# Kernel optimization log

Hardware: AMD Instinct MI355X
Metric: run time of the kernel (lower is better)

## Reference

```python
import jax, jax.numpy as jnp
import numpy as np

NUM_RADII, NUM_THETA = 3, 16
RADIUS = 40.0
DT = 0.1
RELU_SHIFT = 0.2
B, N, NB, T_ENC, OTHER_CH = 4, 512, 512, 16, 3


def _rot_mats():
    # bin-center angles of the num_theta angular bins
    t = (jnp.arange(NUM_THETA, dtype=jnp.float32) + 0.5) * (2.0 * jnp.pi / NUM_THETA) - jnp.pi
    c, s = jnp.cos(t), jnp.sin(t)
    return jnp.stack([jnp.stack([c, -s], -1), jnp.stack([s, c], -1)], -2)  # [T,2,2]


def _steer_kernel(W):
    # W: [R,T,O,I,2,2]; equivariant steering K[r,t] = R(theta_t) W[r,t] R(theta_t)^T
    Rm = _rot_mats()
    K = jnp.einsum('tab,rtoibc,tdc->rtoiad', Rm, W, Rm)
    return K.reshape(NUM_RADII * NUM_THETA, W.shape[2], W.shape[3], 2, 2)  # [K,O,I,2,2]


def _equi_conv(src_pos, qry_pos, feats, mask, W):
    # src_pos [B,S,2], qry_pos [B,Q,2], feats [B,S,I,2] vector features, mask [B,Q,S]
    rel = src_pos[:, None, :, :] - qry_pos[:, :, None, :]          # [B,Q,S,2]
    d2 = jnp.sum(rel * rel, -1)
    dist = jnp.sqrt(d2 + 1e-9)
    theta = jnp.arctan2(rel[..., 1], rel[..., 0])
    rb = jnp.clip((dist / RADIUS * NUM_RADII).astype(jnp.int32), 0, NUM_RADII - 1)
    tb = jnp.mod(jnp.floor((theta + jnp.pi) / (2.0 * jnp.pi) * NUM_THETA).astype(jnp.int32), NUM_THETA)
    kidx = rb * NUM_THETA + tb                                     # [B,Q,S] polar bin id
    win = jnp.maximum(1.0 - d2 / (RADIUS * RADIUS), 0.0) ** 3      # smooth radial window
    w = win * mask
    H = jax.nn.one_hot(kidx, NUM_RADII * NUM_THETA, dtype=feats.dtype) * w[..., None]  # [B,Q,S,K]
    M = jnp.einsum('bqsk,bsiv->bqkiv', H, feats)                   # bin-accumulated neighbor features
    K = _steer_kernel(W)
    return jnp.einsum('bqkiv,koiuv->bqou', M, K)                   # [B,Q,O,2]


def _equi_linear(f, A, Bm):
    # rotation-equivariant linear on vector channels: (a*I + b*J) per (out,in)
    Jf = jnp.stack([-f[..., 1], f[..., 0]], -1)
    return jnp.einsum('oi,bniv->bnov', A, f) + jnp.einsum('oi,bniv->bnov', Bm, Jf)


def _forward(p0_enc, v0_enc, p0, v0, a, other_feats, box, box_feats, fluid_mask, box_mask,
             W_cf, W_co, A_df, B_df, layer_params):
    # update_pos_vel
    v1 = v0 + DT * a
    p1 = p0 + DT * (v0 + v1) * 0.5
    # forward(): feats = cat(other_feats, v0_enc) on channel dim -2
    feats = jnp.concatenate([other_feats, v0_enc], -2)
    # compute_correction
    fluid_feats = jnp.concatenate([v1[:, :, None, :], feats], -2)  # [B,N,20,2]
    out_conv_fluid = _equi_conv(p1, p1, fluid_feats, fluid_mask, W_cf)
    out_dense_fluid = _equi_linear(fluid_feats, A_df, B_df)
    out_conv_obst = _equi_conv(box, p1, box_feats[:, :, None, :], box_mask, W_co)
    output = jnp.concatenate([out_conv_obst, out_conv_fluid, out_dense_fluid], -2)  # [B,N,48,2]
    for (Wc, Ad, Bd) in layer_params:
        mags = (jnp.sum(output * output, -1) + 1e-6)[..., None]
        in_feats = output / mags * jax.nn.relu(mags - RELU_SHIFT)
        oc = _equi_conv(p1, p1, in_feats, fluid_mask, Wc)
        od = _equi_linear(in_feats, Ad, Bd)
        if od.shape[-2] == output.shape[-2]:
            output = oc + od + output
        else:
            output = oc + od
    corr = output / 128.0                                          # [B,N,1,2]
    # apply_correction
    p_corrected = p1 + corr[..., 0, :]
    v_corrected = (p_corrected - p0) / DT
    return p_corrected, v_corrected


def setup_inputs():
    key = jax.random.key(0)
    ks = jax.random.split(key, 32)
    d = {}
    d['p0_enc'] = jax.random.normal(ks[0], (B, N, T_ENC, 2), jnp.float32)
    d['v0_enc'] = jax.random.normal(ks[1], (B, N, T_ENC, 2), jnp.float32)
    d['p0'] = jax.random.uniform(ks[2], (B, N, 2), jnp.float32) * 100.0
    d['v0'] = jax.random.normal(ks[3], (B, N, 2), jnp.float32)
    d['a'] = jax.random.normal(ks[4], (B, N, 2), jnp.float32)
    d['other_feats'] = jax.random.normal(ks[5], (B, N, OTHER_CH, 2), jnp.float32)
    d['box'] = jax.random.uniform(ks[6], (B, NB, 2), jnp.float32) * 100.0
    d['box_feats'] = jax.random.normal(ks[7], (B, NB, 2), jnp.float32)
    d['fluid_mask'] = (jax.random.uniform(ks[8], (B, N, N)) < 0.5).astype(jnp.float32)
    d['box_mask'] = (jax.random.uniform(ks[9], (B, N, NB)) < 0.5).astype(jnp.float32)
    sc = 0.05
    d['W_cf'] = sc * jax.random.normal(ks[10], (NUM_RADII, NUM_THETA, 16, 20, 2, 2), jnp.float32)
    d['W_co'] = sc * jax.random.normal(ks[11], (NUM_RADII, NUM_THETA, 16, 1, 2, 2), jnp.float32)
    d['A_df'] = sc * jax.random.normal(ks[12], (16, 20), jnp.float32)
    d['B_df'] = sc * jax.random.normal(ks[13], (16, 20), jnp.float32)
    chans = [(32, 48), (32, 32), (32, 32), (1, 32)]
    for i, (o, ci) in enumerate(chans, start=1):
        d['W_c%d' % i] = sc * jax.random.normal(ks[13 + 3 * i], (NUM_RADII, NUM_THETA, o, ci, 2, 2), jnp.float32)
        d['A_d%d' % i] = sc * jax.random.normal(ks[14 + 3 * i], (o, ci), jnp.float32)
        d['B_d%d' % i] = sc * jax.random.normal(ks[15 + 3 * i], (o, ci), jnp.float32)
    return d


def reference(p0_enc, v0_enc, p0, v0, a, other_feats, box, box_feats, fluid_mask, box_mask,
              W_cf, W_co, A_df, B_df, W_c1, A_d1, B_d1, W_c2, A_d2, B_d2,
              W_c3, A_d3, B_d3, W_c4, A_d4, B_d4):
    layer_params = [(W_c1, A_d1, B_d1), (W_c2, A_d2, B_d2), (W_c3, A_d3, B_d3), (W_c4, A_d4, B_d4)]
    return _forward(p0_enc, v0_enc, p0, v0, a, other_feats, box, box_feats, fluid_mask, box_mask,
                    W_cf, W_co, A_df, B_df, layer_params)
```

## Files before the change

### kernel.cpp

```cpp
#include <hip/hip_runtime.h>
#include <cstdint>
#include <cstddef>

#define PI_F 3.14159265358979323846f

constexpr int BB = 4, NN = 512, BN = 2048, NBIN = 48;

typedef __attribute__((ext_vector_type(8))) short v8s;
typedef __attribute__((ext_vector_type(4))) float v4f;

__device__ __forceinline__ unsigned short f2bf(float f) {
  unsigned u = __float_as_uint(f);
  unsigned r = (u + 0x7FFFu + ((u >> 16) & 1u)) >> 16;
  return (unsigned short)r;
}
__device__ __forceinline__ float bf2f(unsigned short s) {
  return __uint_as_float(((unsigned)s) << 16);
}

__device__ __forceinline__ void steer_f32(const float* __restrict__ W, float* __restrict__ K2,
                                          int O, int I, int Ipad, int idx, int total) {
  if (idx >= total) return;
  int i = idx % Ipad;
  int o = (idx / Ipad) % O;
  int k = idx / (Ipad * O);
  int CTc = O * 2;
  size_t r0 = (size_t)((k*Ipad + i)*2 + 0) * CTc + o*2;
  size_t r1 = r0 + CTc;
  if (i >= I) { K2[r0]=0.f; K2[r0+1]=0.f; K2[r1]=0.f; K2[r1+1]=0.f; return; }
  int tt = k % 16;
  float ang = (tt + 0.5f) * (2.0f * PI_F / 16.0f) - PI_F;
  float ct = cosf(ang), st = sinf(ang);
  const float* Wp = W + ((size_t)(k*O + o)*I + i) * 4;
  float w00 = Wp[0], w01 = Wp[1], w10 = Wp[2], w11 = Wp[3];
  float rw00 = ct*w00 - st*w10, rw01 = ct*w01 - st*w11;
  float rw10 = st*w00 + ct*w10, rw11 = st*w01 + ct*w11;
  K2[r0 + 0] = rw00*ct - rw01*st;
  K2[r0 + 1] = rw10*ct - rw11*st;
  K2[r1 + 0] = rw00*st + rw01*ct;
  K2[r1 + 1] = rw10*st + rw11*ct;
}

__device__ __forceinline__ void steer_bf16T(const float* __restrict__ W,
                                            unsigned short* __restrict__ K2T,
                                            int O, int I, int Ipad, int Kd,
                                            int idx, int total) {
  if (idx >= total) return;
  int i = idx % Ipad;
  int o = (idx / Ipad) % O;
  int k = idx / (Ipad * O);
  size_t c0 = (size_t)(o*2 + 0) * Kd + (k*Ipad + i)*2;
  size_t c1 = (size_t)(o*2 + 1) * Kd + (k*Ipad + i)*2;
  if (i >= I) { K2T[c0]=0; K2T[c0+1]=0; K2T[c1]=0; K2T[c1+1]=0; return; }
  int tt = k % 16;
  float ang = (tt + 0.5f) * (2.0f * PI_F / 16.0f) - PI_F;
  float ct = cosf(ang), st = sinf(ang);
  const float* Wp = W + ((size_t)(k*O + o)*I + i) * 4;
  float w00 = Wp[0], w01 = Wp[1], w10 = Wp[2], w11 = Wp[3];
  float rw00 = ct*w00 - st*w10, rw01 = ct*w01 - st*w11;
  float rw10 = st*w00 + ct*w10, rw11 = st*w01 + ct*w11;
  K2T[c0 + 0] = f2bf(rw00*ct - rw01*st);
  K2T[c0 + 1] = f2bf(rw00*st + rw01*ct);
  K2T[c1 + 0] = f2bf(rw10*ct - rw11*st);
  K2T[c1 + 1] = f2bf(rw10*st + rw11*ct);
}

__global__ __launch_bounds__(256) void setup_kernel(
    const float* __restrict__ p0, const float* __restrict__ v0,
    const float* __restrict__ a, const float* __restrict__ other,
    const float* __restrict__ v0enc, float* __restrict__ p1, float* __restrict__ F0,
    const float* Wcf, unsigned short* K2CF, const float* Wco, float* K2CO,
    const float* Wc1, unsigned short* K2C1, const float* Wc2, unsigned short* K2C2,
    const float* Wc3, unsigned short* K2C3, const float* Wc4, float* K2C4) {
  int blk = blockIdx.x;
  int t = threadIdx.x;
  if (blk < 8) {
    int n = blk * 256 + t;
    float p0x = p0[n*2], p0y = p0[n*2+1];
    float v0x = v0[n*2], v0y = v0[n*2+1];
    float ax = a[n*2],  ay = a[n*2+1];
    float v1x = v0x + 0.1f*ax, v1y = v0y + 0.1f*ay;
    p1[n*2]   = p0x + 0.1f*(v0x+v1x)*0.5f;
    p1[n*2+1] = p0y + 0.1f*(v0y+v1y)*0.5f;
    float* F = F0 + (size_t)n*48;
    F[0] = v1x; F[1] = v1y;
    for (int c = 0; c < 3; ++c) {
      F[2+c*2]   = other[(n*3+c)*2];
      F[2+c*2+1] = other[(n*3+c)*2+1];
    }
    for (int c = 0; c < 16; ++c) {
      F[8+c*2]   = v0enc[(n*16+c)*2];
      F[8+c*2+1] = v0enc[(n*16+c)*2+1];
    }
    for (int c = 40; c < 48; ++c) F[c] = 0.0f;
  } else if (blk < 80)  steer_bf16T(Wcf, K2CF, 16, 20, 24, 2304, (blk-8)*256 + t, 18432);
  else if (blk < 83)  steer_f32(Wco, K2CO, 16, 1, 1,   (blk-80)*256 + t, 768);
  else if (blk < 371) steer_bf16T(Wc1, K2C1, 32, 48, 48, 4608, (blk-83)*256 + t, 73728);
  else if (blk < 563) steer_bf16T(Wc2, K2C2, 32, 32, 32, 3072, (blk-371)*256 + t, 49152);
  else if (blk < 755) steer_bf16T(Wc3, K2C3, 32, 32, 32, 3072, (blk-563)*256 + t, 49152);
  else                steer_f32(Wc4, K2C4, 1, 32, 32,  (blk-755)*256 + t, 1536);
}

__global__ __launch_bounds__(256) void pairs_all(const float* __restrict__ qry,
                                                 const float* __restrict__ srcF,
                                                 const float* __restrict__ maskF,
                                                 float* __restrict__ wlF, int* __restrict__ plF,
                                                 int* __restrict__ cntF,
                                                 const float* __restrict__ srcO,
                                                 const float* __restrict__ maskO,
                                                 float* __restrict__ wlO, int* __restrict__ plO,
                                                 int* __restrict__ cntO) {
  __shared__ int hist[4][48];
  __shared__ int bstart[4][48];
  __shared__ int runc[4][48];
  bool isBox = blockIdx.x >= 512;
  int qblk = isBox ? (blockIdx.x - 512) : blockIdx.x;
  const float* src = isBox ? srcO : srcF;
  const float* mask = isBox ? maskO : maskF;
  float* wlist = isBox ? wlO : wlF;
  int* plist = isBox ? plO : plF;
  int* cnt = isBox ? cntO : cntF;

  int wv = threadIdx.x >> 6;
  int lane = threadIdx.x & 63;
  int q = qblk * 4 + wv;
  int b = q >> 9;
  float qx = qry[q*2], qy = qry[q*2+1];
  const float* sb = src + b*1024;
  const float* mb = mask + (size_t)q*512;
  float* wl = wlist + (size_t)q*512;
  int* pl = plist + (size_t)q*512;

  if (lane < 48) { hist[wv][lane] = 0; runc[wv][lane] = 0; }

  float wreg[8]; int kreg[8];
  unsigned char predreg[8];
  for (int ch = 0; ch < 8; ++ch) {
    int s = ch*64 + lane;
    float sx = sb[s*2], sy = sb[s*2+1];
    float rx = sx - qx, ry = sy - qy;
    float d2 = rx*rx + ry*ry;
    float m = mb[s];
    float wi = fmaxf(1.0f - d2 / 1600.0f, 0.0f);
    float w = wi*wi*wi*m;
    bool pred = w > 0.0f;
    int k = 63;
    if (pred) {
      float dist = sqrtf(d2 + 1e-9f);
      float theta = atan2f(ry, rx);
      int rb = (int)(dist / 40.0f * 3.0f);
      rb = rb > 2 ? 2 : rb;
      float u = (theta + PI_F) / (2.0f * PI_F) * 16.0f;
      int tb = ((int)floorf(u)) & 15;
      k = rb*16 + tb;
      atomicAdd(&hist[wv][k], 1);
    }
    wreg[ch] = w; kreg[ch] = k; predreg[ch] = pred ? 1 : 0;
  }
  int cntv = (lane < 48) ? hist[wv][lane] : 0;
  int sc = cntv;
  #pragma unroll
  for (int off = 1; off < 64; off <<= 1) {
    int o = __shfl_up(sc, off);
    if (lane >= off) sc += o;
  }
  if (lane < 48) bstart[wv][lane] = sc - cntv;
  if (lane == 47) cnt[q] = sc;

  for (int ch = 0; ch < 8; ++ch) {
    bool pred = predreg[ch] != 0;
    int k = kreg[ch];
    float w = wreg[ch];
    unsigned long long mEq = __ballot(pred);
    #pragma unroll
    for (int bit = 0; bit < 6; ++bit) {
      unsigned long long mbm = __ballot((k >> bit) & 1);
      mEq &= ((k >> bit) & 1) ? mbm : ~mbm;
    }
    int rank = __popcll(mEq & ((1ull<<lane)-1ull));
    int total = __popcll(mEq);
    if (pred) {
      int bs = bstart[wv][k];
      int rc = runc[wv][k];
      int pos = bs + rc + rank;
      int s = ch*64 + lane;
      wl[pos] = w;
      pl[pos] = (s<<6) | k;
      if (rank == total - 1) runc[wv][k] = rc + total;
    }
  }
}

template<int C2>
__device__ __forceinline__ void accum_loop(float* __restrict__ M, int sw, int c, int nnz,
    const float* __restrict__ wls, const int* __restrict__ pls,
    const float* __restrict__ fb) {
  if (nnz <= 0) return;
  constexpr int W = 16;
  float wA[W], fA[W]; int kA[W];
  #pragma unroll
  for (int j = 0; j < W; ++j) {
    bool v = j < nnz;
    float wv = v ? wls[j] : 0.0f;
    int p = v ? pls[j] : 47;
    wA[j] = wv; kA[j] = p & 63;
    fA[j] = fb[(p >> 6) * C2];
  }
  int kcur = -1;
  float acc = 0.0f;
  for (int base = 0; base < nnz; base += W) {
    float wB[W], fB[W]; int kB[W];
    if (base + W < nnz) {
      #pragma unroll
      for (int j = 0; j < W; ++j) {
        int idx = base + W + j;
        bool v = idx < nnz;
        float wv = v ? wls[idx] : 0.0f;
        int p = v ? pls[idx] : 47;
        wB[j] = wv; kB[j] = p & 63;
        fB[j] = fb[(size_t)(p >> 6) * C2];
      }
    }
    asm volatile("" ::: "memory");
    #pragma unroll
    for (int j = 0; j < W; ++j) {
      acc = (kA[j] == kcur ? acc : 0.0f) + wA[j] * fA[j];
      kcur = kA[j];
      M[(kcur * C2 + c) ^ sw] = acc;
    }
    #pragma unroll
    for (int j = 0; j < W; ++j) { wA[j] = wB[j]; kA[j] = kB[j]; fA[j] = fB[j]; }
  }
}

template<int QB, int TPB>
__device__ __forceinline__ void stage_lists(int q0, const int* __restrict__ csh,
    const float* __restrict__ wlist, const int* __restrict__ plist,
    float* __restrict__ wsh, int* __restrict__ psh) {
  const int t = threadIdx.x;
  for (int i = t; i < QB*128; i += TPB) {
    int qs = i >> 7, j = i & 127;
    if (j*4 < csh[qs]) {
      ((float4*)(wsh + qs*512))[j] = ((const float4*)(wlist + (size_t)(q0+qs)*512))[j];
      ((int4*)(psh + qs*512))[j]   = ((const int4*)(plist + (size_t)(q0+qs)*512))[j];
    }
  }
}

template<int C2, int QB, int TPB>
__global__ __launch_bounds__(TPB, 1) void accum4(const float* __restrict__ wlist,
                                                 const int* __restrict__ plist,
                                                 const int* __restrict__ cnt,
                                                 const float* __restrict__ feats,
                                                 unsigned short* __restrict__ Mout) {
  constexpr int Kd = NBIN * C2;
  static_assert(TPB == QB * C2, "TPB must equal QB*C2");
  __shared__ float Ml[QB * Kd];
  __shared__ float wsh[QB*512];
  __shared__ int   psh[QB*512];
  __shared__ int   csh[QB];
  const int t = threadIdx.x;
  const int q0 = blockIdx.x * QB;
  for (int i = t; i < QB*Kd; i += TPB) Ml[i] = 0.0f;
  if (t < QB) csh[t] = (q0 + t < BN) ? cnt[q0 + t] : 0;
  __syncthreads();
  stage_lists<QB, TPB>(q0, csh, wlist, plist, wsh, psh);
  __syncthreads();
  {
    const int ql = t / C2, c = t % C2;
    const int q = q0 + ql;
    accum_loop<C2>(Ml + ql*Kd, 0, c, csh[ql],
                   wsh + ql*512, psh + ql*512,
                   feats + (size_t)(q >> 9)*512*C2 + c);
  }
  __syncthreads();
  const int rows = (q0 + QB <= BN) ? QB : (BN - q0);
  unsigned* dst = (unsigned*)(Mout + (size_t)q0 * Kd);
  const float2* s2 = (const float2*)Ml;
  const int lim = rows * (Kd/2);
  for (int i = t; i < lim; i += TPB) {
    float2 v = s2[i];
    dst[i] = (unsigned)f2bf(v.x) | ((unsigned)f2bf(v.y) << 16);
  }
}

template<int CT>
__global__ __launch_bounds__(256) void gemm_mfma(const unsigned short* __restrict__ A,
                                                 const unsigned short* __restrict__ B,
                                                 float* __restrict__ G, int Kd, int kn) {
  const int lane = threadIdx.x & 63;
  const int w = threadIdx.x >> 6;
  const int mblk = blockIdx.x;
  const int ks = blockIdx.y * 4 + w;
  const int k0 = ks * kn;
  const int m = lane & 15, quad = lane >> 4;
  constexpr int NT = CT / 16;
  const unsigned short* Ar0 = A + (size_t)(mblk*32 + m) * Kd + k0 + quad*8;
  const unsigned short* Ar1 = Ar0 + (size_t)16 * Kd;
  const unsigned short* Bp[NT];
  #pragma unroll
  for (int nt = 0; nt < NT; ++nt)
    Bp[nt] = B + (size_t)(nt*16 + m) * Kd + k0 + quad*8;
  v4f acc[2][NT];
  #pragma unroll
  for (int mt = 0; mt < 2; ++mt)
    for (int nt = 0; nt < NT; ++nt)
      acc[mt][nt] = (v4f){0.0f, 0.0f, 0.0f, 0.0f};
  for (int kt = 0; kt < kn; kt += 32) {
    v8s a0 = *(const v8s*)(Ar0 + kt);
    v8s a1 = *(const v8s*)(Ar1 + kt);
    #pragma unroll
    for (int nt = 0; nt < NT; ++nt) {
      v8s bv = *(const v8s*)(Bp[nt] + kt);
      acc[0][nt] = __builtin_amdgcn_mfma_f32_16x16x32_bf16(a0, bv, acc[0][nt], 0, 0, 0);
      acc[1][nt] = __builtin_amdgcn_mfma_f32_16x16x32_bf16(a1, bv, acc[1][nt], 0, 0, 0);
    }
  }
  float* Gb = G + ((size_t)ks * BN + mblk*32) * CT;
  #pragma unroll
  for (int mt = 0; mt < 2; ++mt)
    for (int nt = 0; nt < NT; ++nt)
      for (int r = 0; r < 4; ++r)
        Gb[(mt*16 + quad*4 + r) * CT + nt*16 + m] = acc[mt][nt][r];
}

__global__ void epilogueL(const float* __restrict__ Gp, int SPLIT,
                          const float* __restrict__ inPrev, int I,
                          const float* __restrict__ Ad, const float* __restrict__ Bd,
                          const float* __restrict__ prevOut, int doRes,
                          float* __restrict__ outCur, float* __restrict__ inNext) {
  int idx = blockIdx.x * blockDim.x + threadIdx.x;
  if (idx >= BN*32) return;
  int o = idx % 32, q = idx / 32;
  float x = 0.0f, y = 0.0f;
  for (int sp = 0; sp < SPLIT; ++sp) {
    size_t base = ((size_t)sp*BN + q)*64 + o*2;
    x += Gp[base]; y += Gp[base+1];
  }
  const float* f = inPrev + (size_t)q * I * 2;
  for (int i = 0; i < I; ++i) {
    float fx = f[i*2], fy = f[i*2+1];
    float Av = Ad[o*I+i], Bv = Bd[o*I+i];
    x += Av*fx - Bv*fy;
    y += Av*fy + Bv*fx;
  }
  if (doRes) {
    x += prevOut[(size_t)idx*2];
    y += prevOut[(size_t)idx*2+1];
  }
  outCur[(size_t)idx*2]   = x;
  outCur[(size_t)idx*2+1] = y;
  float m = x*x + y*y + 1e-6f;
  float sc = fmaxf(m - 0.2f, 0.0f) / m;
  inNext[(size_t)idx*2]   = x * sc;
  inNext[(size_t)idx*2+1] = y * sc;
}

__global__ __launch_bounds__(256, 1) void fused_s0(
    const float* __restrict__ wlF, const int* __restrict__ plF, const int* __restrict__ cntF,
    const float* __restrict__ F0, const unsigned short* __restrict__ K2CF,
    const float* __restrict__ wlO, const int* __restrict__ plO, const int* __restrict__ cntO,
    const float* __restrict__ boxf, const float* __restrict__ K2CO,
    const float* __restrict__ Adf, const float* __restrict__ Bdf,
    float* __restrict__ in1) {
  constexpr int QB = 4;
  constexpr int Kd = 2304;
  constexpr int KW = 576;
  __shared__ float Ml[QB * Kd];
  __shared__ float Mo[QB * 96];
  __shared__ float red[4][QB * 32];
  __shared__ float wshF[QB*512];
  __shared__ int   pshF[QB*512];
  __shared__ float wshO[QB*512];
  __shared__ int   pshO[QB*512];
  __shared__ int cshF[QB];
  __shared__ int cshO[QB];
  const int t = threadIdx.x;
  const int q0 = blockIdx.x * QB;
  for (int i = t; i < QB*Kd; i += 256) Ml[i] = 0.0f;
  for (int i = t; i < QB*96; i += 256) Mo[i] = 0.0f;
  if (t < QB) cshF[t] = cntF[q0 + t];
  else if (t < 2*QB) cshO[t-QB] = cntO[q0 + t - QB];
  __syncthreads();
  for (int i = t; i < 2*QB*128; i += 256) {
    int half = i >> 9;
    int qs = (i >> 7) & (QB-1), j = i & 127;
    if (half == 0) {
      if (j*4 < cshF[qs]) {
        ((float4*)(wshF + qs*512))[j] = ((const float4*)(wlF + (size_t)(q0+qs)*512))[j];
        ((int4*)(pshF + qs*512))[j]   = ((const int4*)(plF + (size_t)(q0+qs)*512))[j];
      }
    } else {
      if (j*4 < cshO[qs]) {
        ((float4*)(wshO + qs*512))[j] = ((const float4*)(wlO + (size_t)(q0+qs)*512))[j];
        ((int4*)(pshO + qs*512))[j]   = ((const int4*)(plO + (size_t)(q0+qs)*512))[j];
      }
    }
  }
  __syncthreads();
  if (t < 192) {
    const int ql = t / 48, c = t % 48;
    const int q = q0 + ql;
    accum_loop<48>(Ml + ql*Kd, (ql & 3) << 2, c, cshF[ql],
                   wshF + ql*512, pshF + ql*512,
                   F0 + (size_t)(q >> 9)*512*48 + c);
  } else if (t < 200) {
    const int idx = t - 192;
    const int ql = idx >> 1, c = idx & 1;
    const int q = q0 + ql;
    accum_loop<2>(Mo + ql*96, 0, c, cshO[ql],
                  wshO + ql*512, pshO + ql*512,
                  boxf + (size_t)(q >> 9)*1024 + c);
  }
  __syncthreads();
  {
    const int lane = t & 63, w = t >> 6;
    const int m = lane & 15, quad = lane >> 4;
    const int ar = m & 3;
    const int sw = ar << 2;
    const float* Abase = Ml + ar * Kd;
    const int kb = w * KW + quad * 8;
    const unsigned short* Bb0 = K2CF + (size_t)m * Kd + kb;
    const unsigned short* Bb1 = K2CF + (size_t)(16 + m) * Kd + kb;
    v4f acc[2];
    acc[0] = (v4f){0,0,0,0}; acc[1] = (v4f){0,0,0,0};
    float4 a0c = *(const float4*)(Abase + (kb ^ sw));
    float4 a1c = *(const float4*)(Abase + ((kb + 4) ^ sw));
    v8s b0c = *(const v8s*)(Bb0);
    v8s b1c = *(const v8s*)(Bb1);
    for (int kt = 0; kt < KW; kt += 32) {
      float4 a0n, a1n; v8s b0n, b1n;
      if (kt + 32 < KW) {
        const int jn = kb + kt + 32;
        a0n = *(const float4*)(Abase + (jn ^ sw));
        a1n = *(const float4*)(Abase + ((jn + 4) ^ sw));
        b0n = *(const v8s*)(Bb0 + kt + 32);
        b1n = *(const v8s*)(Bb1 + kt + 32);
      }
      v8s av;
      av[0]=(short)f2bf(a0c.x); av[1]=(short)f2bf(a0c.y); av[2]=(short)f2bf(a0c.z); av[3]=(short)f2bf(a0c.w);
      av[4]=(short)f2bf(a1c.x); av[5]=(short)f2bf(a1c.y); av[6]=(short)f2bf(a1c.z); av[7]=(short)f2bf(a1c.w);
      acc[0] = __builtin_amdgcn_mfma_f32_16x16x32_bf16(av, b0c, acc[0], 0, 0, 0);
      acc[1] = __builtin_amdgcn_mfma_f32_16x16x32_bf16(av, b1c, acc[1], 0, 0, 0);
      a0c = a0n; a1c = a1n; b0c = b0n; b1c = b1n;
    }
    if (quad == 0) {
      #pragma unroll
      for (int nt = 0; nt < 2; ++nt)
        #pragma unroll
        for (int r = 0; r < 4; ++r)
          red[w][r*32 + nt*16 + m] = acc[nt][r];
    }
  }
  __syncthreads();
  if (t < 192) {
    const int ql = t / 48, ch = t % 48;
    const int q = q0 + ql;
    float x = 0.0f, y = 0.0f;
    if (ch < 16) {
      const float* Mq = Mo + ql*96;
      for (int j = 0; j < 96; ++j) {
        float mv = Mq[j];
        x += mv * K2CO[j*32 + ch*2];
        y += mv * K2CO[j*32 + ch*2 + 1];
      }
    } else if (ch < 32) {
      int o = ch - 16;
      x = red[0][ql*32+o*2] + red[1][ql*32+o*2] + red[2][ql*32+o*2] + red[3][ql*32+o*2];
      y = red[0][ql*32+o*2+1] + red[1][ql*32+o*2+1] + red[2][ql*32+o*2+1] + red[3][ql*32+o*2+1];
    } else {
      int o = ch - 32;
      const float* f = F0 + (size_t)q*48;
      for (int i = 0; i < 20; ++i) {
        float fx = f[i*2], fy = f[i*2+1];
        float Av = Adf[o*20+i], Bv = Bdf[o*20+i];
        x += Av*fx - Bv*fy;
        y += Av*fy + Bv*fx;
      }
    }
    float mm = x*x + y*y + 1e-6f;
    float sc = fmaxf(mm - 0.2f, 0.0f) / mm;
    size_t idx = (size_t)q*48 + ch;
    in1[idx*2]   = x * sc;
    in1[idx*2+1] = y * sc;
  }
}

template<int C2, int CT, int I, int QB>
__global__ __launch_bounds__(C2*QB, 1) void fused_layer(
    const float* __restrict__ wlist, const int* __restrict__ plist,
    const int* __restrict__ cnt, const float* __restrict__ feats,
    const unsigned short* __restrict__ K2T,
    const float* __restrict__ Ad, const float* __restrict__ Bd,
    const float* __restrict__ prevOut, int doRes,
    float* __restrict__ outCur, float* __restrict__ inNext) {
  constexpr int Kd = NBIN * C2;
  constexpr int TPB = C2 * QB;
  constexpr int NW = TPB / 64;
  constexpr int KW = Kd / NW;
  constexpr int NT = CT / 16;
  static_assert(KW % 32 == 0, "KW must be multiple of 32");
  __shared__ float Ml[QB * Kd];
  __shared__ float red[NW][QB * CT];
  __shared__ float wsh[QB*512];
  __shared__ int   psh[QB*512];
  __shared__ int csh[QB];
  const int t = threadIdx.x;
  const int q0 = blockIdx.x * QB;
  for (int i = t; i < QB*Kd; i += TPB) Ml[i] = 0.0f;
  if (t < QB) csh[t] = cnt[q0 + t];
  __syncthreads();
  stage_lists<QB, TPB>(q0, csh, wlist, plist, wsh, psh);
  __syncthreads();
  {
    const int ql = t / C2, c = t % C2;
    const int q = q0 + ql;
    accum_loop<C2>(Ml + ql*Kd, (ql & 3) << 2, c, csh[ql],
                   wsh + ql*512, psh + ql*512,
                   feats + (size_t)(q >> 9)*512*C2 + c);
  }
  __syncthreads();
  const int lane = t & 63, w = t >> 6;
  const int m = lane & 15, quad = lane >> 4;
  const int ar = m & (QB-1);
  const int sw = ar << 2;
  const float* Abase = Ml + ar * Kd;
  const int kb = w * KW + quad * 8;
  const unsigned short* Bb[NT];
  #pragma unroll
  for (int nt = 0; nt < NT; ++nt)
    Bb[nt] = K2T + (size_t)(nt*16 + m) * Kd + kb;
  v4f acc[NT];
  #pragma unroll
  for (int nt = 0; nt < NT; ++nt) acc[nt] = (v4f){0,0,0,0};
  float4 a0c = *(const float4*)(Abase + (kb ^ sw));
  float4 a1c = *(const float4*)(Abase + ((kb + 4) ^ sw));
  v8s bc[NT];
  #pragma unroll
  for (int nt = 0; nt < NT; ++nt) bc[nt] = *(const v8s*)(Bb[nt]);
  for (int kt = 0; kt < KW; kt += 32) {
    float4 a0n, a1n; v8s bn[NT];
    if (kt + 32 < KW) {
      const int jn = kb + kt + 32;
      a0n = *(const float4*)(Abase + (jn ^ sw));
      a1n = *(const float4*)(Abase + ((jn + 4) ^ sw));
      #pragma unroll
      for (int nt = 0; nt < NT; ++nt) bn[nt] = *(const v8s*)(Bb[nt] + kt + 32);
    }
    v8s av;
    av[0]=(short)f2bf(a0c.x); av[1]=(short)f2bf(a0c.y); av[2]=(short)f2bf(a0c.z); av[3]=(short)f2bf(a0c.w);
    av[4]=(short)f2bf(a1c.x); av[5]=(short)f2bf(a1c.y); av[6]=(short)f2bf(a1c.z); av[7]=(short)f2bf(a1c.w);
    #pragma unroll
    for (int nt = 0; nt < NT; ++nt)
      acc[nt] = __builtin_amdgcn_mfma_f32_16x16x32_bf16(av, bc[nt], acc[nt], 0, 0, 0);
    a0c = a0n; a1c = a1n;
    #pragma unroll
    for (int nt = 0; nt < NT; ++nt) bc[nt] = bn[nt];
  }
  if (quad == 0) {
    #pragma unroll
    for (int nt = 0; nt < NT; ++nt)
      #pragma unroll
      for (int r = 0; r < QB; ++r)
        red[w][r*CT + nt*16 + m] = acc[nt][r];
  }
  __syncthreads();
  if (t < QB * (CT/2)) {
    const int o = t % (CT/2), ql = t / (CT/2);
    const int q = q0 + ql;
    float x = 0.0f, y = 0.0f;
    #pragma unroll
    for (int w2 = 0; w2 < NW; ++w2) {
      x += red[w2][ql*CT + o*2];
      y += red[w2][ql*CT + o*2 + 1];
    }
    const float* f = feats + (size_t)q * C2;
    for (int i = 0; i < I; ++i) {
      float fx = f[i*2], fy = f[i*2+1];
      float Av = Ad[o*I + i], Bv = Bd[o*I + i];
      x += Av*fx - Bv*fy;
      y += Av*fy + Bv*fx;
    }
    size_t idx = (size_t)q * (CT/2) + o;
    if (doRes) { x += prevOut[idx*2]; y += prevOut[idx*2+1]; }
    outCur[idx*2]   = x;
    outCur[idx*2+1] = y;
    float mm = x*x + y*y + 1e-6f;
    float sc = fmaxf(mm - 0.2f, 0.0f) / mm;
    inNext[idx*2]   = x * sc;
    inNext[idx*2+1] = y * sc;
  }
}

__global__ __launch_bounds__(256, 1) void fused_l4(
    const float* __restrict__ wl, const int* __restrict__ pl, const int* __restrict__ cnt,
    const float* __restrict__ in4, const float* __restrict__ K2C4,
    const float* __restrict__ Ad4, const float* __restrict__ Bd4,
    const float* __restrict__ p1, const float* __restrict__ p0,
    float* __restrict__ dout) {
  constexpr int QB = 4, Kd = 3072;
  __shared__ float Ml[QB * Kd];
  __shared__ float wsh[QB*512];
  __shared__ int   psh[QB*512];
  __shared__ int csh[QB];
  const int t = threadIdx.x;
  const int q0 = blockIdx.x * QB;
  for (int i = t; i < QB*Kd; i += 256) Ml[i] = 0.0f;
  if (t < QB) csh[t] = cnt[q0 + t];
  __syncthreads();
  stage_lists<QB, 256>(q0, csh, wl, pl, wsh, psh);
  __syncthreads();
  {
    const int ql = t / 64, c = t % 64;
    const int q = q0 + ql;
    accum_loop<64>(Ml + ql*Kd, (ql & 3) << 2, c, csh[ql],
                   wsh + ql*512, psh + ql*512,
                   in4 + (size_t)(q >> 9)*512*64 + c);
  }
  __syncthreads();
  const int lane = t & 63, w = t >> 6;
  const int q = q0 + w;
  const int sw = (w & 3) << 2;
  const float* Mq = Ml + w*Kd;
  float a0 = 0.0f, a1 = 0.0f;
  for (int j = lane; j < Kd; j += 64) {
    float av = Mq[j ^ sw];
    a0 += av * K2C4[j*2];
    a1 += av * K2C4[j*2+1];
  }
  if (lane < 32) {
    float fx = in4[q*64 + lane*2], fy = in4[q*64 + lane*2 + 1];
    float Av = Ad4[lane], Bv = Bd4[lane];
    a0 += Av*fx - Bv*fy;
    a1 += Av*fy + Bv*fx;
  }
  for (int off = 32; off > 0; off >>= 1) {
    a0 += __shfl_down(a0, off);
    a1 += __shfl_down(a1, off);
  }
  if (lane == 0) {
    float px = p1[q*2]   + a0/128.0f;
    float py = p1[q*2+1] + a1/128.0f;
    dout[q*2] = px; dout[q*2+1] = py;
    dout[4096 + q*2]   = (px - p0[q*2]) / 0.1f;
    dout[4096 + q*2+1] = (py - p0[q*2+1]) / 0.1f;
  }
}

extern "C" void kernel_launch(void* const* d_in, const int* in_sizes, int n_in,
                              void* d_out, int out_size, void* d_ws, size_t ws_size,
                              hipStream_t stream) {
  (void)in_sizes; (void)n_in; (void)out_size; (void)ws_size;
  const float* v0_enc = (const float*)d_in[1];
  const float* p0     = (const float*)d_in[2];
  const float* v0     = (const float*)d_in[3];
  const float* a      = (const float*)d_in[4];
  const float* other  = (const float*)d_in[5];
  const float* box    = (const float*)d_in[6];
  const float* boxf   = (const float*)d_in[7];
  const float* fmask  = (const float*)d_in[8];
  const float* bmask  = (const float*)d_in[9];
  const float* Wcf = (const float*)d_in[10];
  const float* Wco = (const float*)d_in[11];
  const float* Adf = (const float*)d_in[12];
  const float* Bdf = (const float*)d_in[13];
  const float* Wc1 = (const float*)d_in[14];
  const float* Ad1 = (const float*)d_in[15];
  const float* Bd1 = (const float*)d_in[16];
  const float* Wc2 = (const float*)d_in[17];
  const float* Ad2 = (const float*)d_in[18];
  const float* Bd2 = (const float*)d_in[19];
  const float* Wc3 = (const float*)d_in[20];
  const float* Ad3 = (const float*)d_in[21];
  const float* Bd3 = (const float*)d_in[22];
  const float* Wc4 = (const float*)d_in[23];
  const float* Ad4 = (const float*)d_in[24];
  const float* Bd4 = (const float*)d_in[25];

  float* ws = (float*)d_ws;
  float* P1    = ws + 0;
  float* F0    = ws + 4096;
  unsigned short* K2CF = (unsigned short*)(ws + 102400);
  float* K2CO  = ws + 176128;
  unsigned short* K2C1 = (unsigned short*)(ws + 179200);
  unsigned short* K2C2 = (unsigned short*)(ws + 474112);
  unsigned short* K2C3 = (unsigned short*)(ws + 670720);
  float* K2C4  = ws + 867328;
  float* WFl   = ws + 873472;
  int*   PFl   = (int*)(ws + 1922048);
  int*   CNTF  = (int*)(ws + 2970624);
  int*   CNTO  = (int*)(ws + 2972672);
  float* IN1   = ws + 2974720;
  float* IN2   = ws + 3171328;
  float* IN3   = ws + 3302400;
  float* IN4   = ws + 3433472;
  float* OUTA  = ws + 3564544;
  float* OUTB  = ws + 3695616;
  float* GPART = ws + 4027392;
  unsigned short* MBUF = (unsigned short*)(ws + 6124544);
  float* WOl   = ws + 15561728;
  int*   POl   = (int*)(ws + 16610304);

  setup_kernel<<<761, 256, 0, stream>>>(p0, v0, a, other, v0_enc, P1, F0,
                                        Wcf, K2CF, Wco, K2CO, Wc1, K2C1,
                                        Wc2, K2C2, Wc3, K2C3, Wc4, K2C4);
  pairs_all<<<1024, 256, 0, stream>>>(P1, P1, fmask, WFl, PFl, CNTF,
                                      box, bmask, WOl, POl, CNTO);
  fused_s0<<<512, 256, 0, stream>>>(WFl, PFl, CNTF, F0, K2CF,
                                    WOl, POl, CNTO, boxf, K2CO, Adf, Bdf, IN1);
  accum4<96, 2, 192><<<1024, 192, 0, stream>>>(WFl, PFl, CNTF, IN1, MBUF);
  gemm_mfma<64><<<dim3(64, 4), 256, 0, stream>>>(MBUF, K2C1, GPART, 4608, 288);
  epilogueL<<<256, 256, 0, stream>>>(GPART, 16, IN1, 48, Ad1, Bd1, nullptr, 0, OUTA, IN2);
  fused_layer<64, 64, 32, 4><<<512, 256, 0, stream>>>(WFl, PFl, CNTF, IN2, K2C2,
                                                      Ad2, Bd2, OUTA, 1, OUTB, IN3);
  fused_layer<64, 64, 32, 4><<<512, 256, 0, stream>>>(WFl, PFl, CNTF, IN3, K2C3,
                                                      Ad3, Bd3, OUTB, 1, OUTA, IN4);
  fused_l4<<<512, 256, 0, stream>>>(WFl, PFl, CNTF, IN4, K2C4, Ad4, Bd4,
                                    P1, p0, (float*)d_out);
}
```

Before: 312.6 us.

## Split each query's sorted pair list across two thread groups and halve queries per block

Each query's bin-sorted neighbour list is split at a bin boundary found by binary search, so two thread groups accumulate disjoint bin ranges of the same query in parallel. Queries per block drop from 4 to 2 (1 for accum4) and grid sizes double, with padded shared-memory rows so the two halves' sentinel writes land in a spare bin. The aim is to shorten the serial accumulation chain and raise parallelism, at the cost of less reuse of the MFMA B operand per block, extra syncs and reduction in fused_l4, and load imbalance when the split is uneven.

```diff
diff --git a/kernel.cpp b/kernel.cpp
--- a/kernel.cpp
+++ b/kernel.cpp
@@ -191,33 +191,48 @@
   }
 }
 
+__device__ __forceinline__ int find_split(const int* __restrict__ pls, int nnz) {
+  if (nnz <= 0) return 0;
+  int kmid = pls[nnz >> 1] & 63;
+  int lo = nnz >> 1, hi = nnz;
+  while (lo < hi) {
+    int m2 = (lo + hi) >> 1;
+    if ((pls[m2] & 63) > kmid) hi = m2; else lo = m2 + 1;
+  }
+  return lo;
+}
+
 template<int C2>
-__device__ __forceinline__ void accum_loop(float* __restrict__ M, int sw, int c, int nnz,
+__device__ __forceinline__ void accum_range(float* __restrict__ M, int sw, int c,
+    int jbeg, int jend,
     const float* __restrict__ wls, const int* __restrict__ pls,
     const float* __restrict__ fb) {
-  if (nnz <= 0) return;
+  int len = jend - jbeg;
+  if (len <= 0) return;
+  const float* wp = wls + jbeg;
+  const int* pp = pls + jbeg;
   constexpr int W = 16;
   float wA[W], fA[W]; int kA[W];
   #pragma unroll
   for (int j = 0; j < W; ++j) {
-    bool v = j < nnz;
-    float wv = v ? wls[j] : 0.0f;
-    int p = v ? pls[j] : 47;
-    wA[j] = wv; kA[j] = p & 63;
+    bool v = j < len;
+    float wv = v ? wp[j] : 0.0f;
+    int p = v ? pp[j] : 0;
+    wA[j] = wv; kA[j] = v ? (p & 63) : 48;
     fA[j] = fb[(p >> 6) * C2];
   }
   int kcur = -1;
   float acc = 0.0f;
-  for (int base = 0; base < nnz; base += W) {
+  for (int base = 0; base < len; base += W) {
     float wB[W], fB[W]; int kB[W];
-    if (base + W < nnz) {
+    if (base + W < len) {
       #pragma unroll
       for (int j = 0; j < W; ++j) {
         int idx = base + W + j;
-        bool v = idx < nnz;
-        float wv = v ? wls[idx] : 0.0f;
-        int p = v ? pls[idx] : 47;
-        wB[j] = wv; kB[j] = p & 63;
+        bool v = idx < len;
+        float wv = v ? wp[idx] : 0.0f;
+        int p = v ? pp[idx] : 0;
+        wB[j] = wv; kB[j] = v ? (p & 63) : 48;
         fB[j] = fb[(size_t)(p >> 6) * C2];
       }
     }
@@ -247,38 +262,44 @@
   }
 }
 
-template<int C2, int QB, int TPB>
+template<int C2, int TPB>
 __global__ __launch_bounds__(TPB, 1) void accum4(const float* __restrict__ wlist,
                                                  const int* __restrict__ plist,
                                                  const int* __restrict__ cnt,
                                                  const float* __restrict__ feats,
                                                  unsigned short* __restrict__ Mout) {
   constexpr int Kd = NBIN * C2;
-  static_assert(TPB == QB * C2, "TPB must equal QB*C2");
-  __shared__ float Ml[QB * Kd];
-  __shared__ float wsh[QB*512];
-  __shared__ int   psh[QB*512];
-  __shared__ int   csh[QB];
+  constexpr int KdP = Kd + C2;
+  static_assert(TPB == 2 * C2, "TPB must equal 2*C2");
+  __shared__ float Ml[KdP];
+  __shared__ float wsh[512];
+  __shared__ int   psh[512];
+  __shared__ int   csh[1];
   const int t = threadIdx.x;
-  const int q0 = blockIdx.x * QB;
-  for (int i = t; i < QB*Kd; i += TPB) Ml[i] = 0.0f;
-  if (t < QB) csh[t] = (q0 + t < BN) ? cnt[q0 + t] : 0;
-  __syncthreads();
-  stage_lists<QB, TPB>(q0, csh, wlist, plist, wsh, psh);
+  const int q = blockIdx.x;
+  for (int i = t; i < KdP; i += TPB) Ml[i] = 0.0f;
+  if (t == 0) csh[0] = cnt[q];
   __syncthreads();
   {
-    const int ql = t / C2, c = t % C2;
-    const int q = q0 + ql;
-    accum_loop<C2>(Ml + ql*Kd, 0, c, csh[ql],
-                   wsh + ql*512, psh + ql*512,
-                   feats + (size_t)(q >> 9)*512*C2 + c);
-  }
-  __syncthreads();
-  const int rows = (q0 + QB <= BN) ? QB : (BN - q0);
-  unsigned* dst = (unsigned*)(Mout + (size_t)q0 * Kd);
+    for (int i = t; i < 128; i += TPB) {
+      if (i*4 < csh[0]) {
+        ((float4*)wsh)[i] = ((const float4*)(wlist + (size_t)q*512))[i];
+        ((int4*)psh)[i]   = ((const int4*)(plist + (size_t)q*512))[i];
+      }
+    }
+  }
+  __syncthreads();
+  {
+    const int half = t / C2, c = t % C2;
+    const int nnz = csh[0];
+    const int js = find_split(psh, nnz);
+    accum_range<C2>(Ml, 0, c, half ? js : 0, half ? nnz : js,
+                    wsh, psh, feats + (size_t)(q >> 9)*512*C2 + c);
+  }
+  __syncthreads();
+  unsigned* dst = (unsigned*)(Mout + (size_t)q * Kd);
   const float2* s2 = (const float2*)Ml;
-  const int lim = rows * (Kd/2);
-  for (int i = t; i < lim; i += TPB) {
+  for (int i = t; i < Kd/2; i += TPB) {
     float2 v = s2[i];
     dst[i] = (unsigned)f2bf(v.x) | ((unsigned)f2bf(v.y) << 16);
   }
@@ -363,11 +384,12 @@
     const float* __restrict__ boxf, const float* __restrict__ K2CO,
     const float* __restrict__ Adf, const float* __restrict__ Bdf,
     float* __restrict__ in1) {
-  constexpr int QB = 4;
+  constexpr int QB = 2;
   constexpr int Kd = 2304;
+  constexpr int KdP = 2352;
   constexpr int KW = 576;
-  __shared__ float Ml[QB * Kd];
-  __shared__ float Mo[QB * 96];
+  __shared__ float Ml[QB * KdP];
+  __shared__ float Mo[QB * 98];
   __shared__ float red[4][QB * 32];
   __shared__ float wshF[QB*512];
   __shared__ int   pshF[QB*512];
@@ -377,14 +399,14 @@
   __shared__ int cshO[QB];
   const int t = threadIdx.x;
   const int q0 = blockIdx.x * QB;
-  for (int i = t; i < QB*Kd; i += 256) Ml[i] = 0.0f;
-  for (int i = t; i < QB*96; i += 256) Mo[i] = 0.0f;
+  for (int i = t; i < QB*KdP; i += 256) Ml[i] = 0.0f;
+  for (int i = t; i < QB*98; i += 256) Mo[i] = 0.0f;
   if (t < QB) cshF[t] = cntF[q0 + t];
   else if (t < 2*QB) cshO[t-QB] = cntO[q0 + t - QB];
   __syncthreads();
   for (int i = t; i < 2*QB*128; i += 256) {
-    int half = i >> 9;
-    int qs = (i >> 7) & (QB-1), j = i & 127;
+    int half = i / (QB*128);
+    int qs = (i / 128) % QB, j = i % 128;
     if (half == 0) {
       if (j*4 < cshF[qs]) {
         ((float4*)(wshF + qs*512))[j] = ((const float4*)(wlF + (size_t)(q0+qs)*512))[j];
@@ -399,26 +421,32 @@
   }
   __syncthreads();
   if (t < 192) {
-    const int ql = t / 48, c = t % 48;
+    const int grp = t / 48, c = t % 48;
+    const int ql = grp >> 1, half = grp & 1;
     const int q = q0 + ql;
-    accum_loop<48>(Ml + ql*Kd, (ql & 3) << 2, c, cshF[ql],
-                   wshF + ql*512, pshF + ql*512,
-                   F0 + (size_t)(q >> 9)*512*48 + c);
+    const int nnz = cshF[ql];
+    const int js = find_split(pshF + ql*512, nnz);
+    accum_range<48>(Ml + ql*KdP, ql << 2, c, half ? js : 0, half ? nnz : js,
+                    wshF + ql*512, pshF + ql*512,
+                    F0 + (size_t)(q >> 9)*512*48 + c);
   } else if (t < 200) {
     const int idx = t - 192;
-    const int ql = idx >> 1, c = idx & 1;
+    const int grp = idx >> 1, c = idx & 1;
+    const int ql = grp >> 1, half = grp & 1;
     const int q = q0 + ql;
-    accum_loop<2>(Mo + ql*96, 0, c, cshO[ql],
-                  wshO + ql*512, pshO + ql*512,
-                  boxf + (size_t)(q >> 9)*1024 + c);
+    const int nnz = cshO[ql];
+    const int js = find_split(pshO + ql*512, nnz);
+    accum_range<2>(Mo + ql*98, 0, c, half ? js : 0, half ? nnz : js,
+                   wshO + ql*512, pshO + ql*512,
+                   boxf + (size_t)(q >> 9)*1024 + c);
   }
   __syncthreads();
   {
     const int lane = t & 63, w = t >> 6;
     const int m = lane & 15, quad = lane >> 4;
-    const int ar = m & 3;
+    const int ar = m & 1;
     const int sw = ar << 2;
-    const float* Abase = Ml + ar * Kd;
+    const float* Abase = Ml + ar * KdP;
     const int kb = w * KW + quad * 8;
     const unsigned short* Bb0 = K2CF + (size_t)m * Kd + kb;
     const unsigned short* Bb1 = K2CF + (size_t)(16 + m) * Kd + kb;
@@ -448,17 +476,17 @@
       #pragma unroll
       for (int nt = 0; nt < 2; ++nt)
         #pragma unroll
-        for (int r = 0; r < 4; ++r)
+        for (int r = 0; r < QB; ++r)
           red[w][r*32 + nt*16 + m] = acc[nt][r];
     }
   }
   __syncthreads();
-  if (t < 192) {
+  if (t < QB*48) {
     const int ql = t / 48, ch = t % 48;
     const int q = q0 + ql;
     float x = 0.0f, y = 0.0f;
     if (ch < 16) {
-      const float* Mq = Mo + ql*96;
+      const float* Mq = Mo + ql*98;
       for (int j = 0; j < 96; ++j) {
         float mv = Mq[j];
         x += mv * K2CO[j*32 + ch*2];
@@ -486,45 +514,50 @@
   }
 }
 
-template<int C2, int CT, int I, int QB>
-__global__ __launch_bounds__(C2*QB, 1) void fused_layer(
+template<int C2, int CT, int I>
+__global__ __launch_bounds__(C2*4, 1) void fused_layer(
     const float* __restrict__ wlist, const int* __restrict__ plist,
     const int* __restrict__ cnt, const float* __restrict__ feats,
     const unsigned short* __restrict__ K2T,
     const float* __restrict__ Ad, const float* __restrict__ Bd,
     const float* __restrict__ prevOut, int doRes,
     float* __restrict__ outCur, float* __restrict__ inNext) {
+  constexpr int QB = 2;
   constexpr int Kd = NBIN * C2;
-  constexpr int TPB = C2 * QB;
+  constexpr int KdP = Kd + C2;
+  constexpr int TPB = C2 * 4;
   constexpr int NW = TPB / 64;
   constexpr int KW = Kd / NW;
   constexpr int NT = CT / 16;
   static_assert(KW % 32 == 0, "KW must be multiple of 32");
-  __shared__ float Ml[QB * Kd];
+  __shared__ float Ml[QB * KdP];
   __shared__ float red[NW][QB * CT];
   __shared__ float wsh[QB*512];
   __shared__ int   psh[QB*512];
   __shared__ int csh[QB];
   const int t = threadIdx.x;
   const int q0 = blockIdx.x * QB;
-  for (int i = t; i < QB*Kd; i += TPB) Ml[i] = 0.0f;
+  for (int i = t; i < QB*KdP; i += TPB) Ml[i] = 0.0f;
   if (t < QB) csh[t] = cnt[q0 + t];
   __syncthreads();
   stage_lists<QB, TPB>(q0, csh, wlist, plist, wsh, psh);
   __syncthreads();
   {
-    const int ql = t / C2, c = t % C2;
+    const int grp = t / C2, c = t % C2;
+    const int ql = grp >> 1, half = grp & 1;
     const int q = q0 + ql;
-    accum_loop<C2>(Ml + ql*Kd, (ql & 3) << 2, c, csh[ql],
-                   wsh + ql*512, psh + ql*512,
-                   feats + (size_t)(q >> 9)*512*C2 + c);
+    const int nnz = csh[ql];
+    const int js = find_split(psh + ql*512, nnz);
+    accum_range<C2>(Ml + ql*KdP, ql << 2, c, half ? js : 0, half ? nnz : js,
+                    wsh + ql*512, psh + ql*512,
+                    feats + (size_t)(q >> 9)*512*C2 + c);
   }
   __syncthreads();
   const int lane = t & 63, w = t >> 6;
   const int m = lane & 15, quad = lane >> 4;
-  const int ar = m & (QB-1);
+  const int ar = m & 1;
   const int sw = ar << 2;
-  const float* Abase = Ml + ar * Kd;
+  const float* Abase = Ml + ar * KdP;
   const int kb = w * KW + quad * 8;
   const unsigned short* Bb[NT];
   #pragma unroll
@@ -598,37 +631,42 @@
     const float* __restrict__ Ad4, const float* __restrict__ Bd4,
     const float* __restrict__ p1, const float* __restrict__ p0,
     float* __restrict__ dout) {
-  constexpr int QB = 4, Kd = 3072;
-  __shared__ float Ml[QB * Kd];
+  constexpr int QB = 2, Kd = 3072, KdP = 3136;
+  __shared__ float Ml[QB * KdP];
   __shared__ float wsh[QB*512];
   __shared__ int   psh[QB*512];
   __shared__ int csh[QB];
+  __shared__ float r4[QB][2][2];
   const int t = threadIdx.x;
   const int q0 = blockIdx.x * QB;
-  for (int i = t; i < QB*Kd; i += 256) Ml[i] = 0.0f;
+  for (int i = t; i < QB*KdP; i += 256) Ml[i] = 0.0f;
   if (t < QB) csh[t] = cnt[q0 + t];
   __syncthreads();
   stage_lists<QB, 256>(q0, csh, wl, pl, wsh, psh);
   __syncthreads();
   {
-    const int ql = t / 64, c = t % 64;
+    const int grp = t / 64, c = t % 64;
+    const int ql = grp >> 1, half = grp & 1;
     const int q = q0 + ql;
-    accum_loop<64>(Ml + ql*Kd, (ql & 3) << 2, c, csh[ql],
-                   wsh + ql*512, psh + ql*512,
-                   in4 + (size_t)(q >> 9)*512*64 + c);
+    const int nnz = csh[ql];
+    const int js = find_split(psh + ql*512, nnz);
+    accum_range<64>(Ml + ql*KdP, ql << 2, c, half ? js : 0, half ? nnz : js,
+                    wsh + ql*512, psh + ql*512,
+                    in4 + (size_t)(q >> 9)*512*64 + c);
   }
   __syncthreads();
   const int lane = t & 63, w = t >> 6;
-  const int q = q0 + w;
-  const int sw = (w & 3) << 2;
-  const float* Mq = Ml + w*Kd;
+  const int ql = w >> 1, kh = w & 1;
+  const int q = q0 + ql;
+  const int sw = ql << 2;
+  const float* Mq = Ml + ql*KdP;
   float a0 = 0.0f, a1 = 0.0f;
-  for (int j = lane; j < Kd; j += 64) {
+  for (int j = kh*1536 + lane; j < kh*1536 + 1536; j += 64) {
     float av = Mq[j ^ sw];
     a0 += av * K2C4[j*2];
     a1 += av * K2C4[j*2+1];
   }
-  if (lane < 32) {
+  if (kh == 0 && lane < 32) {
     float fx = in4[q*64 + lane*2], fy = in4[q*64 + lane*2 + 1];
     float Av = Ad4[lane], Bv = Bd4[lane];
     a0 += Av*fx - Bv*fy;
@@ -638,12 +676,17 @@
     a0 += __shfl_down(a0, off);
     a1 += __shfl_down(a1, off);
   }
-  if (lane == 0) {
-    float px = p1[q*2]   + a0/128.0f;
-    float py = p1[q*2+1] + a1/128.0f;
-    dout[q*2] = px; dout[q*2+1] = py;
-    dout[4096 + q*2]   = (px - p0[q*2]) / 0.1f;
-    dout[4096 + q*2+1] = (py - p0[q*2+1]) / 0.1f;
+  if (lane == 0) { r4[ql][kh][0] = a0; r4[ql][kh][1] = a1; }
+  __syncthreads();
+  if (t < QB) {
+    int qq = q0 + t;
+    float s0 = r4[t][0][0] + r4[t][1][0];
+    float s1 = r4[t][0][1] + r4[t][1][1];
+    float px = p1[qq*2]   + s0/128.0f;
+    float py = p1[qq*2+1] + s1/128.0f;
+    dout[qq*2] = px; dout[qq*2+1] = py;
+    dout[4096 + qq*2]   = (px - p0[qq*2]) / 0.1f;
+    dout[4096 + qq*2+1] = (py - p0[qq*2+1]) / 0.1f;
   }
 }
 
@@ -706,15 +749,15 @@
                                         Wc2, K2C2, Wc3, K2C3, Wc4, K2C4);
   pairs_all<<<1024, 256, 0, stream>>>(P1, P1, fmask, WFl, PFl, CNTF,
                                       box, bmask, WOl, POl, CNTO);
-  fused_s0<<<512, 256, 0, stream>>>(WFl, PFl, CNTF, F0, K2CF,
-                                    WOl, POl, CNTO, boxf, K2CO, Adf, Bdf, IN1);
-  accum4<96, 2, 192><<<1024, 192, 0, stream>>>(WFl, PFl, CNTF, IN1, MBUF);
+  fused_s0<<<1024, 256, 0, stream>>>(WFl, PFl, CNTF, F0, K2CF,
+                                     WOl, POl, CNTO, boxf, K2CO, Adf, Bdf, IN1);
+  accum4<96, 192><<<2048, 192, 0, stream>>>(WFl, PFl, CNTF, IN1, MBUF);
   gemm_mfma<64><<<dim3(64, 4), 256, 0, stream>>>(MBUF, K2C1, GPART, 4608, 288);
   epilogueL<<<256, 256, 0, stream>>>(GPART, 16, IN1, 48, Ad1, Bd1, nullptr, 0, OUTA, IN2);
-  fused_layer<64, 64, 32, 4><<<512, 256, 0, stream>>>(WFl, PFl, CNTF, IN2, K2C2,
-                                                      Ad2, Bd2, OUTA, 1, OUTB, IN3);
-  fused_layer<64, 64, 32, 4><<<512, 256, 0, stream>>>(WFl, PFl, CNTF, IN3, K2C3,
-                                                      Ad3, Bd3, OUTB, 1, OUTA, IN4);
-  fused_l4<<<512, 256, 0, stream>>>(WFl, PFl, CNTF, IN4, K2C4, Ad4, Bd4,
-                                    P1, p0, (float*)d_out);
-}
+  fused_layer<64, 64, 32><<<1024, 256, 0, stream>>>(WFl, PFl, CNTF, IN2, K2C2,
+                                                    Ad2, Bd2, OUTA, 1, OUTB, IN3);
+  fused_layer<64, 64, 32><<<1024, 256, 0, stream>>>(WFl, PFl, CNTF, IN3, K2C3,
+                                                    Ad3, Bd3, OUTB, 1, OUTA, IN4);
+  fused_l4<<<1024, 256, 0, stream>>>(WFl, PFl, CNTF, IN4, K2C4, Ad4, Bd4,
+                                     P1, p0, (float*)d_out);
+}
```

After: 356.7 us. +14.1%, slower.
